# Kernel optimization log

Hardware: AMD Instinct MI355X
Metric: run time of the kernel (lower is better)

Reference implementation:

```python
import jax, jax.numpy as jnp
import numpy as np

# Layer dims and sparsity levels, hard-coded in the original module
_DIMS = [(1024, 1000, 0.73), (1000, 800, 0.72), (800, 400, 0.70), (400, 600, 0.70), (600, 6, 0.50)]


def setup_inputs() -> dict:
    key = jax.random.key(0)
    ks = jax.random.split(key, 1 + 3 * len(_DIMS))
    inp = {"x": jax.random.normal(ks[0], (32768, 1024), dtype=jnp.float32)}
    for i, (fin, fout, sp) in enumerate(_DIMS):
        kw, kb, km = ks[1 + 3 * i], ks[2 + 3 * i], ks[3 + 3 * i]
        # Kaiming-ish init like nn.Linear default
        bound = 1.0 / np.sqrt(fin)
        inp[f"W{i+1}"] = jax.random.uniform(kw, (fout, fin), jnp.float32, -bound, bound)
        inp[f"b{i+1}"] = jax.random.uniform(kb, (fout,), jnp.float32, -bound, bound)
        # Unstructured sparsity mask: fraction `sp` of weights are zero
        inp[f"mask{i+1}"] = (jax.random.uniform(km, (fout, fin)) >= sp)
    return inp


def _sparse_linear(x, W, b, mask):
    # y = x @ (W * mask)^T + b ; mask encodes the fixed sparse connectivity
    Ws = jnp.where(mask, W, 0.0)
    return x @ Ws.T + b


def reference(x, W1, b1, mask1, W2, b2, mask2, W3, b3, mask3, W4, b4, mask4, W5, b5, mask5):
    h1 = jax.nn.relu(_sparse_linear(x, W1, b1, mask1))   # [B, 1000]
    h2 = jax.nn.relu(_sparse_linear(h1, W2, b2, mask2))  # [B, 800]
    h3 = jax.nn.relu(_sparse_linear(h2, W3, b3, mask3))  # [B, 400]
    h4 = _sparse_linear(h3, W4, b4, mask4)               # [B, 600] (no relu)
    h5 = _sparse_linear(h4, W5, b5, mask5)               # [B, 6]   (no relu)
    # original returns (x, results dict); return tuple (final, fc1..fc5)
    return (h5, h1, h2, h3, h4, h5)
```

## Files before the change

### kernel.cpp

```cpp
#include <hip/hip_runtime.h>
#include <stdint.h>

using u8  = unsigned char;
using u16 = unsigned short;
using u32 = unsigned int;

typedef __bf16 bf16x8 __attribute__((ext_vector_type(8)));
typedef float  f32x4  __attribute__((ext_vector_type(4)));

__device__ __forceinline__ float b2f(u16 u) {
    union { u32 i; float f; } v; v.i = ((u32)u) << 16; return v.f;
}
__device__ __forceinline__ u16 f2bf(float f) {
    union { float f; u32 i; } v; v.f = f;
    u32 u = v.i;
    return (u16)((u + 0x7FFFu + ((u >> 16) & 1u)) >> 16);
}

#define WS_OFF 256
#define OFF_W1 0
#define OFF_W2 1048576
#define OFF_W3 1966080
#define OFF_W4 2392064
#define PS1 1048576
#define PS2 917504
#define PS3 425984
#define PS4 286720

__global__ void detect_kernel(int* __restrict__ flags,
                              const u32* __restrict__ xw,
                              const u32* __restrict__ mw) {
    const int lane = threadIdx.x;
    int outl = 0;
#pragma unroll
    for (int i = 0; i < 4; ++i) {
        u32 u = xw[lane * 4 + i];
        u32 e = (u >> 7) & 0xFFu;
        if (e < 90u || e > 140u) outl++;
    }
#pragma unroll
    for (int off = 32; off; off >>= 1) outl += __shfl_down(outl, off, 64);

    u32 v0 = mw[lane], v1 = mw[64 + lane];
    bool w4 = (v0 == 0u || v0 == 1u || v0 == 0x3F800000u) &&
              (v1 == 0u || v1 == 1u || v1 == 0x3F800000u);
    auto okh = [](u32 h) { return h == 0u || h == 1u || h == 0x3F80u; };
    bool w2 = okh(v0 & 0xFFFFu) && okh(v0 >> 16) && okh(v1 & 0xFFFFu) && okh(v1 >> 16);
    int all4 = __all(w4 ? 1 : 0);
    int all2 = __all(w2 ? 1 : 0);
    if (lane == 0) {
        flags[0] = (outl > 64) ? 1 : 0;
        flags[1] = all4 ? 0 : (all2 ? 1 : 2);
    }
}

__device__ __forceinline__ bool readM(const void* m, int s, int mwid) {
    if (mwid == 0) return ((const u32*)m)[s] != 0u;
    if (mwid == 1) return ((const u16*)m)[s] != 0u;
    return ((const u8*)m)[s] != 0u;
}
__device__ __forceinline__ u16 readW(const void* W, int s, int dt) {
    if (dt) return f2bf(((const float*)W)[s]);
    return ((const u16*)W)[s];
}

__global__ void prep_weights(const int* __restrict__ flags, u16* __restrict__ ws,
                             const void* __restrict__ W1, const void* __restrict__ m1,
                             const void* __restrict__ W2, const void* __restrict__ m2,
                             const void* __restrict__ W3, const void* __restrict__ m3,
                             const void* __restrict__ W4, const void* __restrict__ m4)
{
    const int dt = flags[0], mwid = flags[1];
    int idx = blockIdx.x * 256 + threadIdx.x;
    if (idx < PS1) {
        int n = idx >> 10, k = idx & 1023;
        u16 v = 0;
        if (n < 1000) { int s = n * 1024 + k; if (readM(m1, s, mwid)) v = readW(W1, s, dt); }
        ws[idx] = v;
    } else if (idx < PS1 + PS2) {
        int j = idx - PS1; int n = j >> 10, k = j & 1023;
        u16 v = 0;
        if (n < 800 && k < 1000) { int s = n * 1000 + k; if (readM(m2, s, mwid)) v = readW(W2, s, dt); }
        ws[idx] = v;
    } else if (idx < PS1 + PS2 + PS3) {
        int j = idx - (PS1 + PS2); int n = j / 832, k = j - n * 832;
        u16 v = 0;
        if (n < 400 && k < 800) { int s = n * 800 + k; if (readM(m3, s, mwid)) v = readW(W3, s, dt); }
        ws[idx] = v;
    } else if (idx < PS1 + PS2 + PS3 + PS4) {
        int j = idx - (PS1 + PS2 + PS3); int n = j / 448, k = j - n * 448;
        u16 v = 0;
        if (n < 600 && k < 400) { int s = n * 400 + k; if (readM(m4, s, mwid)) v = readW(W4, s, dt); }
        ws[idx] = v;
    }
}

template <bool RELU, int MODE>
__global__ __launch_bounds__(256, 3) void gemm_bt(
    const int* __restrict__ flags,
    const void* __restrict__ Av, int strideA, int Kpad,
    const u16* __restrict__ Wp,
    const void* __restrict__ biasv, int N,
    void* __restrict__ Cv)
{
    if (flags[0] != MODE) return;

    __shared__ __attribute__((aligned(16))) char sA[32768];
    __shared__ __attribute__((aligned(16))) char sB[16384];

    const int tid  = threadIdx.x;
    const int lane = tid & 63, wid = tid >> 6;
    const int wm = wid >> 1, wn = wid & 1;
    const int bm0 = blockIdx.x * 128, bn0 = blockIdx.y * 128;
    const int q = lane >> 4, r15 = lane & 15, key = lane & 7;

    const int l3 = lane >> 3, l7 = lane & 7;
    const int kbxB = ((l7 ^ l3) << 3);
    const u16* gB = Wp + (size_t)(bn0 + wid * 32 + l3) * (size_t)Kpad + kbxB;
    char* sBw = sB + wid * 4096;

    const u16*  gA16 = nullptr;
    const float* gAf = nullptr;
    char* sAw;
    if constexpr (MODE == 0) {
        gA16 = (const u16*)Av + (size_t)(bm0 + wid * 32 + l3) * (size_t)strideA + kbxB;
        sAw = sA + wid * 4096;
    } else {
        gAf = (const float*)Av + (size_t)bm0 * (size_t)strideA;
        sAw = sA + wid * 8192;
    }

    f32x4 acc[4][4];
#pragma unroll
    for (int i = 0; i < 4; ++i)
#pragma unroll
        for (int j = 0; j < 4; ++j) acc[i][j] = (f32x4){0.f, 0.f, 0.f, 0.f};

    for (int k0 = 0; k0 < Kpad; k0 += 64) {
        if (k0) __syncthreads();
        if constexpr (MODE == 0) {
#pragma unroll
            for (int t = 0; t < 4; ++t)
                __builtin_amdgcn_global_load_lds(
                    (const __attribute__((address_space(1))) void*)(gA16 + (size_t)t * 8 * strideA),
                    (__attribute__((address_space(3))) void*)(sAw + t * 1024), 16, 0, 0);
            gA16 += 64;
        } else {
            const int l4 = lane >> 4, c = lane & 15;
#pragma unroll
            for (int t = 0; t < 8; ++t) {
                int rl = wid * 32 + t * 4 + l4;
                int cg = c ^ (rl & 15);
                const float* src = gAf + (size_t)rl * strideA + k0 + cg * 4;
                __builtin_amdgcn_global_load_lds(
                    (const __attribute__((address_space(1))) void*)src,
                    (__attribute__((address_space(3))) void*)(sAw + t * 1024), 16, 0, 0);
            }
        }
#pragma unroll
        for (int t = 0; t < 4; ++t)
            __builtin_amdgcn_global_load_lds(
                (const __attribute__((address_space(1))) void*)(gB + (size_t)t * 8 * Kpad),
                (__attribute__((address_space(3))) void*)(sBw + t * 1024), 16, 0, 0);
        gB += 64;
        __syncthreads();

#pragma unroll
        for (int kk = 0; kk < 2; ++kk) {
            bf16x8 af[4], bfr[4];
#pragma unroll
            for (int mi = 0; mi < 4; ++mi) {
                if constexpr (MODE == 0) {
                    af[mi] = *(const bf16x8*)(sA + (wm * 64 + mi * 16 + r15) * 128 +
                                              (((kk * 4 + q) ^ key) << 4));
                } else {
                    int r = wm * 64 + mi * 16 + r15;
                    int j2 = (kk * 4 + q) * 2;
                    f32x4 a0 = *(const f32x4*)(sA + r * 256 + ((j2 ^ (r & 15)) << 4));
                    f32x4 a1 = *(const f32x4*)(sA + r * 256 + (((j2 + 1) ^ (r & 15)) << 4));
                    bf16x8 tv;
                    tv[0] = (__bf16)a0[0]; tv[1] = (__bf16)a0[1];
                    tv[2] = (__bf16)a0[2]; tv[3] = (__bf16)a0[3];
                    tv[4] = (__bf16)a1[0]; tv[5] = (__bf16)a1[1];
                    tv[6] = (__bf16)a1[2]; tv[7] = (__bf16)a1[3];
                    af[mi] = tv;
                }
            }
#pragma unroll
            for (int ni = 0; ni < 4; ++ni)
                bfr[ni] = *(const bf16x8*)(sB + (wn * 64 + ni * 16 + r15) * 128 +
                                           (((kk * 4 + q) ^ key) << 4));
#pragma unroll
            for (int mi = 0; mi < 4; ++mi)
#pragma unroll
                for (int ni = 0; ni < 4; ++ni)
                    acc[mi][ni] = __builtin_amdgcn_mfma_f32_16x16x32_bf16(
                        af[mi], bfr[ni], acc[mi][ni], 0, 0, 0);
        }
    }

    float bv[4];
#pragma unroll
    for (int ni = 0; ni < 4; ++ni) {
        int col = bn0 + wn * 64 + ni * 16 + r15;
        bv[ni] = (col < N) ? (MODE ? ((const float*)biasv)[col] : b2f(((const u16*)biasv)[col]))
                           : 0.f;
    }
#pragma unroll
    for (int mi = 0; mi < 4; ++mi) {
#pragma unroll
        for (int ni = 0; ni < 4; ++ni) {
            int col = bn0 + wn * 64 + ni * 16 + r15;
            if (col < N) {
#pragma unroll
                for (int rr = 0; rr < 4; ++rr) {
                    int row = bm0 + wm * 64 + mi * 16 + q * 4 + rr;
                    float v = acc[mi][ni][rr] + bv[ni];
                    if (RELU) v = v > 0.f ? v : 0.f;
                    if (MODE) ((float*)Cv)[(size_t)row * N + col] = v;
                    else      ((u16*)Cv)[(size_t)row * N + col] = f2bf(v);
                }
            }
        }
    }
}

template <int MODE>
__global__ void layer5(const int* __restrict__ flags,
                       const void* __restrict__ h4v,
                       const void* __restrict__ W5v, const void* __restrict__ b5v,
                       const void* __restrict__ m5v,
                       void* __restrict__ out0v, void* __restrict__ out5v)
{
    if (flags[0] != MODE) return;
    const int mwid = flags[1];
    __shared__ float w[6 * 600];
    __shared__ float bs[6];
    const int tid = threadIdx.x;
    for (int i = tid; i < 3600; i += 256)
        w[i] = readM(m5v, i, mwid)
                 ? (MODE ? ((const float*)W5v)[i] : b2f(((const u16*)W5v)[i])) : 0.f;
    if (tid < 6)
        bs[tid] = MODE ? ((const float*)b5v)[tid] : b2f(((const u16*)b5v)[tid]);
    __syncthreads();

    const int wid = tid >> 6, lane = tid & 63;
    const int row = blockIdx.x * 4 + wid;

    float acc[6] = {0.f, 0.f, 0.f, 0.f, 0.f, 0.f};
    for (int p = lane; p < 300; p += 64) {
        float f0, f1;
        if (MODE) {
            float2 hv = *(const float2*)((const float*)h4v + (size_t)row * 600 + 2 * p);
            f0 = hv.x; f1 = hv.y;
        } else {
            u32 u = *(const u32*)((const u16*)h4v + (size_t)row * 600 + 2 * p);
            f0 = b2f((u16)(u & 0xffff)); f1 = b2f((u16)(u >> 16));
        }
        int k = 2 * p;
#pragma unroll
        for (int j = 0; j < 6; ++j) {
            float2 wv = *(const float2*)&w[j * 600 + k];
            acc[j] += f0 * wv.x + f1 * wv.y;
        }
    }
#pragma unroll
    for (int j = 0; j < 6; ++j)
#pragma unroll
        for (int off = 32; off > 0; off >>= 1)
            acc[j] += __shfl_down(acc[j], off, 64);

    if (lane == 0) {
#pragma unroll
        for (int j = 0; j < 6; ++j) {
            float v = acc[j] + bs[j];
            if (MODE) {
                ((float*)out0v)[(size_t)row * 6 + j] = v;
                ((float*)out5v)[(size_t)row * 6 + j] = v;
            } else {
                u16 b = f2bf(v);
                ((u16*)out0v)[(size_t)row * 6 + j] = b;
                ((u16*)out5v)[(size_t)row * 6 + j] = b;
            }
        }
    }
}

extern "C" void kernel_launch(void* const* d_in, const int* in_sizes, int n_in,
                              void* d_out, int out_size, void* d_ws, size_t ws_size,
                              hipStream_t stream) {
    int* flags = (int*)d_ws;
    u16* wsW   = (u16*)d_ws + WS_OFF;

    detect_kernel<<<1, 64, 0, stream>>>(flags, (const u32*)d_in[0], (const u32*)d_in[3]);
    prep_weights<<<10464, 256, 0, stream>>>(flags, wsW,
                                            d_in[1], d_in[3], d_in[4], d_in[6],
                                            d_in[7], d_in[9], d_in[10], d_in[12]);

    u16*   o16 = (u16*)d_out;
    float* o32 = (float*)d_out;

    gemm_bt<true, 0><<<dim3(256, 8), 256, 0, stream>>>(flags, d_in[0], 1024, 1024,
                                                       wsW + OFF_W1, d_in[2], 1000, o16 + 196608);
    gemm_bt<true, 1><<<dim3(256, 8), 256, 0, stream>>>(flags, d_in[0], 1024, 1024,
                                                       wsW + OFF_W1, d_in[2], 1000, o32 + 196608);
    gemm_bt<true, 0><<<dim3(256, 7), 256, 0, stream>>>(flags, o16 + 196608, 1000, 1024,
                                                       wsW + OFF_W2, d_in[5], 800, o16 + 32964608);
    gemm_bt<true, 1><<<dim3(256, 7), 256, 0, stream>>>(flags, o32 + 196608, 1000, 1024,
                                                       wsW + OFF_W2, d_in[5], 800, o32 + 32964608);
    gemm_bt<true, 0><<<dim3(256, 4), 256, 0, stream>>>(flags, o16 + 32964608, 800, 832,
                                                       wsW + OFF_W3, d_in[8], 400, o16 + 59179008);
    gemm_bt<true, 1><<<dim3(256, 4), 256, 0, stream>>>(flags, o32 + 32964608, 800, 832,
                                                       wsW + OFF_W3, d_in[8], 400, o32 + 59179008);
    gemm_bt<false, 0><<<dim3(256, 5), 256, 0, stream>>>(flags, o16 + 59179008, 400, 448,
                                                        wsW + OFF_W4, d_in[11], 600, o16 + 72286208);
    gemm_bt<false, 1><<<dim3(256, 5), 256, 0, stream>>>(flags, o32 + 59179008, 400, 448,
                                                        wsW + OFF_W4, d_in[11], 600, o32 + 72286208);
    layer5<0><<<8192, 256, 0, stream>>>(flags, o16 + 72286208, d_in[13], d_in[14], d_in[15],
                                        o16, o16 + 91947008);
    layer5<1><<<8192, 256, 0, stream>>>(flags, o32 + 72286208, d_in[13], d_in[14], d_in[15],
                                        o32, o32 + 91947008);
}
```

Baseline: 904.8 us.

## Convert fp32 activations to bf16 workspace copies and unify GEMM launches

```diff
diff --git a/kernel.cpp b/kernel.cpp
--- a/kernel.cpp
+++ b/kernel.cpp
@@ -7,6 +7,7 @@
 
 typedef __bf16 bf16x8 __attribute__((ext_vector_type(8)));
 typedef float  f32x4  __attribute__((ext_vector_type(4)));
+typedef u16    u16x8  __attribute__((ext_vector_type(8)));
 
 __device__ __forceinline__ float b2f(u16 u) {
     union { u32 i; float f; } v; v.i = ((u32)u) << 16; return v.f;
@@ -26,6 +27,13 @@
 #define PS2 917504
 #define PS3 425984
 #define PS4 286720
+#define TOTW 2678784
+#define GUARD 64
+#define OFF_XC  2678784
+#define OFF_H1C 36233216
+#define OFF_H2C 69001280
+#define OFF_H3C 95215744
+#define XCONV_N 4194304
 
 __global__ void detect_kernel(int* __restrict__ flags,
                               const u32* __restrict__ xw,
@@ -68,7 +76,8 @@
                              const void* __restrict__ W1, const void* __restrict__ m1,
                              const void* __restrict__ W2, const void* __restrict__ m2,
                              const void* __restrict__ W3, const void* __restrict__ m3,
-                             const void* __restrict__ W4, const void* __restrict__ m4)
+                             const void* __restrict__ W4, const void* __restrict__ m4,
+                             const void* __restrict__ xv)
 {
     const int dt = flags[0], mwid = flags[1];
     int idx = blockIdx.x * 256 + threadIdx.x;
@@ -87,48 +96,64 @@
         u16 v = 0;
         if (n < 400 && k < 800) { int s = n * 800 + k; if (readM(m3, s, mwid)) v = readW(W3, s, dt); }
         ws[idx] = v;
-    } else if (idx < PS1 + PS2 + PS3 + PS4) {
+    } else if (idx < TOTW) {
         int j = idx - (PS1 + PS2 + PS3); int n = j / 448, k = j - n * 448;
         u16 v = 0;
         if (n < 600 && k < 400) { int s = n * 400 + k; if (readM(m4, s, mwid)) v = readW(W4, s, dt); }
         ws[idx] = v;
-    }
-}
-
-template <bool RELU, int MODE>
+    } else if (idx < TOTW + 3 * GUARD) {
+        int g = idx - TOTW;
+        int zone = g >> 6;
+        size_t off = (zone == 0) ? ((size_t)OFF_H1C + 32768000)
+                   : (zone == 1) ? ((size_t)OFF_H2C + 26214400)
+                                 : ((size_t)OFF_H3C + 13107200);
+        ws[off + (g & 63)] = 0;
+    } else if (dt) {
+        int c = idx - (TOTW + 3 * GUARD);
+        if (c < XCONV_N) {
+            const float4* s = (const float4*)xv + (size_t)c * 2;
+            float4 a = s[0], b = s[1];
+            u16x8 o;
+            o[0] = f2bf(a.x); o[1] = f2bf(a.y); o[2] = f2bf(a.z); o[3] = f2bf(a.w);
+            o[4] = f2bf(b.x); o[5] = f2bf(b.y); o[6] = f2bf(b.z); o[7] = f2bf(b.w);
+            ((u16x8*)(ws + OFF_XC))[c] = o;
+        }
+    }
+}
+
+template <bool RELU>
 __global__ __launch_bounds__(256, 3) void gemm_bt(
     const int* __restrict__ flags,
-    const void* __restrict__ Av, int strideA, int Kpad,
+    const u16* __restrict__ A0,
+    const u16* __restrict__ A1,
+    int strideA, int Kpad, int NY,
     const u16* __restrict__ Wp,
-    const void* __restrict__ biasv, int N,
-    void* __restrict__ Cv)
+    const void* __restrict__ bias, int N,
+    void* __restrict__ dOut, size_t outOff,
+    u16* __restrict__ Cc)
 {
-    if (flags[0] != MODE) return;
-
-    __shared__ __attribute__((aligned(16))) char sA[32768];
+    const int mode = flags[0];
+    const u16* __restrict__ A = mode ? A1 : A0;
+
+    __shared__ __attribute__((aligned(16))) char sA[16384];
     __shared__ __attribute__((aligned(16))) char sB[16384];
 
     const int tid  = threadIdx.x;
     const int lane = tid & 63, wid = tid >> 6;
     const int wm = wid >> 1, wn = wid & 1;
-    const int bm0 = blockIdx.x * 128, bn0 = blockIdx.y * 128;
+
+    const int per = gridDim.x >> 3;
+    const int idx = (blockIdx.x & 7) * per + (blockIdx.x >> 3);
+    const int bm0 = (idx / NY) * 128, bn0 = (idx % NY) * 128;
+
     const int q = lane >> 4, r15 = lane & 15, key = lane & 7;
-
     const int l3 = lane >> 3, l7 = lane & 7;
-    const int kbxB = ((l7 ^ l3) << 3);
-    const u16* gB = Wp + (size_t)(bn0 + wid * 32 + l3) * (size_t)Kpad + kbxB;
+    const int kbx = (l7 ^ l3) << 3;
+
+    const u16* gA = A  + (size_t)(bm0 + wid * 32 + l3) * (size_t)strideA + kbx;
+    const u16* gB = Wp + (size_t)(bn0 + wid * 32 + l3) * (size_t)Kpad   + kbx;
+    char* sAw = sA + wid * 4096;
     char* sBw = sB + wid * 4096;
-
-    const u16*  gA16 = nullptr;
-    const float* gAf = nullptr;
-    char* sAw;
-    if constexpr (MODE == 0) {
-        gA16 = (const u16*)Av + (size_t)(bm0 + wid * 32 + l3) * (size_t)strideA + kbxB;
-        sAw = sA + wid * 4096;
-    } else {
-        gAf = (const float*)Av + (size_t)bm0 * (size_t)strideA;
-        sAw = sA + wid * 8192;
-    }
 
     f32x4 acc[4][4];
 #pragma unroll
@@ -138,54 +163,25 @@
 
     for (int k0 = 0; k0 < Kpad; k0 += 64) {
         if (k0) __syncthreads();
-        if constexpr (MODE == 0) {
-#pragma unroll
-            for (int t = 0; t < 4; ++t)
-                __builtin_amdgcn_global_load_lds(
-                    (const __attribute__((address_space(1))) void*)(gA16 + (size_t)t * 8 * strideA),
-                    (__attribute__((address_space(3))) void*)(sAw + t * 1024), 16, 0, 0);
-            gA16 += 64;
-        } else {
-            const int l4 = lane >> 4, c = lane & 15;
-#pragma unroll
-            for (int t = 0; t < 8; ++t) {
-                int rl = wid * 32 + t * 4 + l4;
-                int cg = c ^ (rl & 15);
-                const float* src = gAf + (size_t)rl * strideA + k0 + cg * 4;
-                __builtin_amdgcn_global_load_lds(
-                    (const __attribute__((address_space(1))) void*)src,
-                    (__attribute__((address_space(3))) void*)(sAw + t * 1024), 16, 0, 0);
-            }
-        }
-#pragma unroll
-        for (int t = 0; t < 4; ++t)
+#pragma unroll
+        for (int t = 0; t < 4; ++t) {
+            __builtin_amdgcn_global_load_lds(
+                (const __attribute__((address_space(1))) void*)(gA + (size_t)t * 8 * strideA),
+                (__attribute__((address_space(3))) void*)(sAw + t * 1024), 16, 0, 0);
             __builtin_amdgcn_global_load_lds(
                 (const __attribute__((address_space(1))) void*)(gB + (size_t)t * 8 * Kpad),
                 (__attribute__((address_space(3))) void*)(sBw + t * 1024), 16, 0, 0);
-        gB += 64;
+        }
+        gA += 64; gB += 64;
         __syncthreads();
 
 #pragma unroll
         for (int kk = 0; kk < 2; ++kk) {
             bf16x8 af[4], bfr[4];
 #pragma unroll
-            for (int mi = 0; mi < 4; ++mi) {
-                if constexpr (MODE == 0) {
-                    af[mi] = *(const bf16x8*)(sA + (wm * 64 + mi * 16 + r15) * 128 +
-                                              (((kk * 4 + q) ^ key) << 4));
-                } else {
-                    int r = wm * 64 + mi * 16 + r15;
-                    int j2 = (kk * 4 + q) * 2;
-                    f32x4 a0 = *(const f32x4*)(sA + r * 256 + ((j2 ^ (r & 15)) << 4));
-                    f32x4 a1 = *(const f32x4*)(sA + r * 256 + (((j2 + 1) ^ (r & 15)) << 4));
-                    bf16x8 tv;
-                    tv[0] = (__bf16)a0[0]; tv[1] = (__bf16)a0[1];
-                    tv[2] = (__bf16)a0[2]; tv[3] = (__bf16)a0[3];
-                    tv[4] = (__bf16)a1[0]; tv[5] = (__bf16)a1[1];
-                    tv[6] = (__bf16)a1[2]; tv[7] = (__bf16)a1[3];
-                    af[mi] = tv;
-                }
-            }
+            for (int mi = 0; mi < 4; ++mi)
+                af[mi] = *(const bf16x8*)(sA + (wm * 64 + mi * 16 + r15) * 128 +
+                                          (((kk * 4 + q) ^ key) << 4));
 #pragma unroll
             for (int ni = 0; ni < 4; ++ni)
                 bfr[ni] = *(const bf16x8*)(sB + (wn * 64 + ni * 16 + r15) * 128 +
@@ -203,9 +199,11 @@
 #pragma unroll
     for (int ni = 0; ni < 4; ++ni) {
         int col = bn0 + wn * 64 + ni * 16 + r15;
-        bv[ni] = (col < N) ? (MODE ? ((const float*)biasv)[col] : b2f(((const u16*)biasv)[col]))
+        bv[ni] = (col < N) ? (mode ? ((const float*)bias)[col] : b2f(((const u16*)bias)[col]))
                            : 0.f;
     }
+    float* out32 = (float*)dOut + outOff;
+    u16*   out16 = (u16*)dOut + outOff;
 #pragma unroll
     for (int mi = 0; mi < 4; ++mi) {
 #pragma unroll
@@ -217,44 +215,45 @@
                     int row = bm0 + wm * 64 + mi * 16 + q * 4 + rr;
                     float v = acc[mi][ni][rr] + bv[ni];
                     if (RELU) v = v > 0.f ? v : 0.f;
-                    if (MODE) ((float*)Cv)[(size_t)row * N + col] = v;
-                    else      ((u16*)Cv)[(size_t)row * N + col] = f2bf(v);
+                    size_t o = (size_t)row * N + col;
+                    if (Cc) Cc[o] = f2bf(v);
+                    if (mode) out32[o] = v;
+                    else      out16[o] = f2bf(v);
                 }
             }
         }
     }
 }
 
-template <int MODE>
-__global__ void layer5(const int* __restrict__ flags,
-                       const void* __restrict__ h4v,
+__global__ void layer5(const int* __restrict__ flags, void* __restrict__ dOut,
                        const void* __restrict__ W5v, const void* __restrict__ b5v,
-                       const void* __restrict__ m5v,
-                       void* __restrict__ out0v, void* __restrict__ out5v)
+                       const void* __restrict__ m5v)
 {
-    if (flags[0] != MODE) return;
-    const int mwid = flags[1];
+    const int mode = flags[0], mwid = flags[1];
     __shared__ float w[6 * 600];
     __shared__ float bs[6];
     const int tid = threadIdx.x;
     for (int i = tid; i < 3600; i += 256)
         w[i] = readM(m5v, i, mwid)
-                 ? (MODE ? ((const float*)W5v)[i] : b2f(((const u16*)W5v)[i])) : 0.f;
+                 ? (mode ? ((const float*)W5v)[i] : b2f(((const u16*)W5v)[i])) : 0.f;
     if (tid < 6)
-        bs[tid] = MODE ? ((const float*)b5v)[tid] : b2f(((const u16*)b5v)[tid]);
+        bs[tid] = mode ? ((const float*)b5v)[tid] : b2f(((const u16*)b5v)[tid]);
     __syncthreads();
 
     const int wid = tid >> 6, lane = tid & 63;
     const int row = blockIdx.x * 4 + wid;
+
+    const float* h4f = (const float*)dOut + 72286208;
+    const u16*   h4b = (const u16*)dOut + 72286208;
 
     float acc[6] = {0.f, 0.f, 0.f, 0.f, 0.f, 0.f};
     for (int p = lane; p < 300; p += 64) {
         float f0, f1;
-        if (MODE) {
-            float2 hv = *(const float2*)((const float*)h4v + (size_t)row * 600 + 2 * p);
+        if (mode) {
+            float2 hv = *(const float2*)(h4f + (size_t)row * 600 + 2 * p);
             f0 = hv.x; f1 = hv.y;
         } else {
-            u32 u = *(const u32*)((const u16*)h4v + (size_t)row * 600 + 2 * p);
+            u32 u = *(const u32*)(h4b + (size_t)row * 600 + 2 * p);
             f0 = b2f((u16)(u & 0xffff)); f1 = b2f((u16)(u >> 16));
         }
         int k = 2 * p;
@@ -274,13 +273,14 @@
 #pragma unroll
         for (int j = 0; j < 6; ++j) {
             float v = acc[j] + bs[j];
-            if (MODE) {
-                ((float*)out0v)[(size_t)row * 6 + j] = v;
-                ((float*)out5v)[(size_t)row * 6 + j] = v;
+            size_t o0 = (size_t)row * 6 + j;
+            if (mode) {
+                ((float*)dOut)[o0] = v;
+                ((float*)dOut)[91947008 + o0] = v;
             } else {
                 u16 b = f2bf(v);
-                ((u16*)out0v)[(size_t)row * 6 + j] = b;
-                ((u16*)out5v)[(size_t)row * 6 + j] = b;
+                ((u16*)dOut)[o0] = b;
+                ((u16*)dOut)[91947008 + o0] = b;
             }
         }
     }
@@ -293,31 +293,22 @@
     u16* wsW   = (u16*)d_ws + WS_OFF;
 
     detect_kernel<<<1, 64, 0, stream>>>(flags, (const u32*)d_in[0], (const u32*)d_in[3]);
-    prep_weights<<<10464, 256, 0, stream>>>(flags, wsW,
+    prep_weights<<<26849, 256, 0, stream>>>(flags, wsW,
                                             d_in[1], d_in[3], d_in[4], d_in[6],
-                                            d_in[7], d_in[9], d_in[10], d_in[12]);
-
-    u16*   o16 = (u16*)d_out;
-    float* o32 = (float*)d_out;
-
-    gemm_bt<true, 0><<<dim3(256, 8), 256, 0, stream>>>(flags, d_in[0], 1024, 1024,
-                                                       wsW + OFF_W1, d_in[2], 1000, o16 + 196608);
-    gemm_bt<true, 1><<<dim3(256, 8), 256, 0, stream>>>(flags, d_in[0], 1024, 1024,
-                                                       wsW + OFF_W1, d_in[2], 1000, o32 + 196608);
-    gemm_bt<true, 0><<<dim3(256, 7), 256, 0, stream>>>(flags, o16 + 196608, 1000, 1024,
-                                                       wsW + OFF_W2, d_in[5], 800, o16 + 32964608);
-    gemm_bt<true, 1><<<dim3(256, 7), 256, 0, stream>>>(flags, o32 + 196608, 1000, 1024,
-                                                       wsW + OFF_W2, d_in[5], 800, o32 + 32964608);
-    gemm_bt<true, 0><<<dim3(256, 4), 256, 0, stream>>>(flags, o16 + 32964608, 800, 832,
-                                                       wsW + OFF_W3, d_in[8], 400, o16 + 59179008);
-    gemm_bt<true, 1><<<dim3(256, 4), 256, 0, stream>>>(flags, o32 + 32964608, 800, 832,
-                                                       wsW + OFF_W3, d_in[8], 400, o32 + 59179008);
-    gemm_bt<false, 0><<<dim3(256, 5), 256, 0, stream>>>(flags, o16 + 59179008, 400, 448,
-                                                        wsW + OFF_W4, d_in[11], 600, o16 + 72286208);
-    gemm_bt<false, 1><<<dim3(256, 5), 256, 0, stream>>>(flags, o32 + 59179008, 400, 448,
-                                                        wsW + OFF_W4, d_in[11], 600, o32 + 72286208);
-    layer5<0><<<8192, 256, 0, stream>>>(flags, o16 + 72286208, d_in[13], d_in[14], d_in[15],
-                                        o16, o16 + 91947008);
-    layer5<1><<<8192, 256, 0, stream>>>(flags, o32 + 72286208, d_in[13], d_in[14], d_in[15],
-                                        o32, o32 + 91947008);
-}
+                                            d_in[7], d_in[9], d_in[10], d_in[12],
+                                            d_in[0]);
+
+    gemm_bt<true><<<2048, 256, 0, stream>>>(flags, (const u16*)d_in[0], wsW + OFF_XC,
+                                            1024, 1024, 8, wsW + OFF_W1, d_in[2], 1000,
+                                            d_out, 196608, wsW + OFF_H1C);
+    gemm_bt<true><<<1792, 256, 0, stream>>>(flags, wsW + OFF_H1C, wsW + OFF_H1C,
+                                            1000, 1024, 7, wsW + OFF_W2, d_in[5], 800,
+                                            d_out, 32964608, wsW + OFF_H2C);
+    gemm_bt<true><<<1024, 256, 0, stream>>>(flags, wsW + OFF_H2C, wsW + OFF_H2C,
+                                            800, 832, 4, wsW + OFF_W3, d_in[8], 400,
+                                            d_out, 59179008, wsW + OFF_H3C);
+    gemm_bt<false><<<1280, 256, 0, stream>>>(flags, wsW + OFF_H3C, wsW + OFF_H3C,
+                                             400, 448, 5, wsW + OFF_W4, d_in[11], 600,
+                                             d_out, 72286208, (u16*)nullptr);
+    layer5<<<8192, 256, 0, stream>>>(flags, d_out, d_in[13], d_in[14], d_in[15]);
+}
```

New measurement: 826.9 us. 1.09x faster.
